# Optimization experiments

Measured on AMD Instinct MI355X. Metric: run time of the kernel, lower is better.

Reference implementation:

```python
import jax, jax.numpy as jnp
import numpy as np

NUM_ITERATIONS = 3

def _squash(s):
    # Original squash reduces over the trailing singleton dim -> elementwise.
    sn = s * s
    return sn * s / ((1.0 + sn) * jnp.sqrt(sn))

def setup_inputs() -> dict:
    key = jax.random.key(0)
    k1, k2 = jax.random.split(key)
    x = jax.random.normal(k1, (128, 1152, 8), dtype=jnp.float32)
    W = jax.random.normal(k2, (1, 1152, 16, 16, 8), dtype=jnp.float32)
    return {"x": x, "W": W}

def reference(x, W):
    # x: [B, R, I]; W: [1, R, C, O, I]
    Wr = W[0]  # [R, C, O, I]
    # u_hat = W @ x broadcast over capsules: [B, R, C, O]
    u_hat = jnp.einsum('rcoi,bri->brco', Wr, x)
    R, C = Wr.shape[0], Wr.shape[1]
    b = jnp.zeros((R, C), dtype=x.dtype)  # routing logits (shared across batch)
    v = None
    for it in range(NUM_ITERATIONS):
        # legacy F.softmax on [1,R,C,1] -> dim=1 == routes axis
        c = jax.nn.softmax(b, axis=0)  # [R, C]
        s = jnp.einsum('rc,brco->bco', c, u_hat)  # [B, C, O]
        v = _squash(s)
        if it < NUM_ITERATIONS - 1:
            # agreement: <u_hat, v> averaged over batch
            a = jnp.einsum('brco,bco->brc', u_hat, v).mean(axis=0)  # [R, C]
            b = b + a
    return v  # [B, C, O] == v_j.squeeze(1).squeeze(-1)
```

## Files before the change

### kernel.cpp

```cpp
#include <hip/hip_runtime.h>
#include <math.h>

#define B_   128
#define R_   1152
#define C_   16
#define O_   16
#define RS_  192
#define RCH_ 6

#define WS_SP   0
#define WS_V    6291456
#define WS_BLOG 6324224
#define WS_CW   6342656
#define WS_AB   6361088

__device__ __forceinline__ float squashf(float s) {
    return s * fabsf(s) / (1.0f + s * s);
}

__global__ void softmax_k(float* __restrict__ blog, const float* __restrict__ ab,
                          float* __restrict__ cw, int first) {
    const int c = blockIdx.x;
    const int t = threadIdx.x;
    __shared__ float red[256];

    float m = -1e30f;
    for (int r = t; r < R_; r += 256) {
        const float prev = first ? 0.f : blog[r * C_ + c];
        const float bl = prev + (ab[r * C_ + c] + ab[R_ * C_ + r * C_ + c]) * (1.0f / (float)B_);
        blog[r * C_ + c] = bl;
        m = fmaxf(m, bl);
    }
    red[t] = m; __syncthreads();
    for (int s = 128; s > 0; s >>= 1) {
        if (t < s) red[t] = fmaxf(red[t], red[t + s]);
        __syncthreads();
    }
    const float M = red[0]; __syncthreads();

    float e = 0.f;
    for (int r = t; r < R_; r += 256) e += __expf(blog[r * C_ + c] - M);
    red[t] = e; __syncthreads();
    for (int s = 128; s > 0; s >>= 1) {
        if (t < s) red[t] += red[t + s];
        __syncthreads();
    }
    const float inv = 1.0f / red[0];

    for (int r = t; r < R_; r += 256)
        cw[r * C_ + c] = __expf(blog[r * C_ + c] - M) * inv;
}

template <bool USECW>
__global__ __launch_bounds__(256) void gemm_s_k(const float* __restrict__ x,
                                                const float* __restrict__ W,
                                                const float* __restrict__ cw,
                                                float* __restrict__ sp) {
    const int bt  = blockIdx.x;
    const int rs  = blockIdx.y;
    const int t   = threadIdx.x;
    const int co4 = t & 63;
    const int b4  = t >> 6;
    const int c   = co4 >> 2;
    const int r0  = rs * RCH_;

    __shared__ float4 wl4[RCH_ * 520];
    __shared__ float4 xl4[16 * 2 * RCH_];

    const float4* __restrict__ X4 = (const float4*)x;
    const float4* __restrict__ W4 = (const float4*)W;

    #pragma unroll
    for (int kk = 0; kk < 12; ++kk) {
        const int u  = t + kk * 256;
        const int rr = u >> 9, j = u & 511;
        wl4[rr * 520 + (j & 7) * 65 + (j >> 3)] = W4[r0 * 512 + u];
    }
    if (t < 192) {
        const int bl = t / 12, rem = t % 12;
        xl4[t] = X4[((bt * 16 + bl) * R_ + r0) * 2 + rem];
    }
    __syncthreads();

    float acc[4][4];
    #pragma unroll
    for (int j = 0; j < 4; ++j)
        #pragma unroll
        for (int q = 0; q < 4; ++q) acc[j][q] = 0.f;

    #pragma unroll
    for (int rr = 0; rr < RCH_; ++rr) {
        const float cwv = USECW ? cw[(r0 + rr) * C_ + c] : (1.0f / (float)R_);
        const int wb = rr * 520 + co4;
        const float4 w0 = wl4[wb +   0], w1 = wl4[wb +  65];
        const float4 w2 = wl4[wb + 130], w3 = wl4[wb + 195];
        const float4 w4 = wl4[wb + 260], w5 = wl4[wb + 325];
        const float4 w6 = wl4[wb + 390], w7 = wl4[wb + 455];
        #pragma unroll
        for (int j = 0; j < 4; ++j) {
            const float4 xa = xl4[(b4 * 4 + j) * 12 + rr * 2];
            const float4 xb = xl4[(b4 * 4 + j) * 12 + rr * 2 + 1];
            const float d0 = w0.x*xa.x + w0.y*xa.y + w0.z*xa.z + w0.w*xa.w
                           + w1.x*xb.x + w1.y*xb.y + w1.z*xb.z + w1.w*xb.w;
            const float d1 = w2.x*xa.x + w2.y*xa.y + w2.z*xa.z + w2.w*xa.w
                           + w3.x*xb.x + w3.y*xb.y + w3.z*xb.z + w3.w*xb.w;
            const float d2 = w4.x*xa.x + w4.y*xa.y + w4.z*xa.z + w4.w*xa.w
                           + w5.x*xb.x + w5.y*xb.y + w5.z*xb.z + w5.w*xb.w;
            const float d3 = w6.x*xa.x + w6.y*xa.y + w6.z*xa.z + w6.w*xa.w
                           + w7.x*xb.x + w7.y*xb.y + w7.z*xb.z + w7.w*xb.w;
            acc[j][0] = fmaf(cwv, d0, acc[j][0]);
            acc[j][1] = fmaf(cwv, d1, acc[j][1]);
            acc[j][2] = fmaf(cwv, d2, acc[j][2]);
            acc[j][3] = fmaf(cwv, d3, acc[j][3]);
        }
    }

    float4* sp4 = (float4*)sp;
    #pragma unroll
    for (int j = 0; j < 4; ++j) {
        const int b = bt * 16 + b4 * 4 + j;
        float4 o4; o4.x = acc[j][0]; o4.y = acc[j][1]; o4.z = acc[j][2]; o4.w = acc[j][3];
        sp4[(rs * B_ + b) * 64 + co4] = o4;
    }
}

__global__ __launch_bounds__(1024) void reduce_squash_k(const float* __restrict__ sp,
                                                        float* __restrict__ outv) {
    const int t   = threadIdx.x;
    const int li  = t & 255;
    const int kq  = t >> 8;
    const int idx = blockIdx.x * 256 + li;
    const float* p = sp + (size_t)kq * (RS_ / 4) * 32768 + idx;
    float a0 = 0.f, a1 = 0.f, a2 = 0.f, a3 = 0.f;
    #pragma unroll 6
    for (int k = 0; k < RS_ / 4; k += 4) {
        a0 += p[(k + 0) * 32768];
        a1 += p[(k + 1) * 32768];
        a2 += p[(k + 2) * 32768];
        a3 += p[(k + 3) * 32768];
    }
    __shared__ float red[1024];
    red[t] = (a0 + a1) + (a2 + a3);
    __syncthreads();
    if (t < 256) {
        const float s = (red[t] + red[t + 256]) + (red[t + 512] + red[t + 768]);
        outv[idx] = squashf(s);
    }
}

__global__ __launch_bounds__(512) void a_k(const float* __restrict__ x,
                                           const float* __restrict__ W,
                                           const float* __restrict__ v,
                                           float* __restrict__ ab) {
    const int rg   = blockIdx.x >> 1;
    const int half = blockIdx.x & 1;
    const int r0   = rg * 4;
    const int b00  = half * 64;
    const int t    = threadIdx.x;
    const int w    = t >> 6, lane = t & 63;
    const int rr   = w & 3, sq = w >> 2;
    const int co4  = lane, c = lane >> 2;

    __shared__ float4 xl[64 * 8];
    __shared__ float4 wl[4 * 520];
    __shared__ float  red[128];
    const float4* __restrict__ X4 = (const float4*)x;
    const float4* __restrict__ V4 = (const float4*)v;
    const float4* __restrict__ W4 = (const float4*)W;

    #pragma unroll
    for (int kk = 0; kk < 4; ++kk) {
        const int u  = t + kk * 512;
        const int r2 = u >> 9, j = u & 511;
        wl[r2 * 520 + (j & 7) * 65 + (j >> 3)] = W4[r0 * 512 + u];
    }
    {
        const int bl = t >> 3, rem = t & 7;
        xl[t] = X4[((b00 + bl) * R_ + r0) * 2 + rem];
    }
    __syncthreads();

    float y[8][4];
    #pragma unroll
    for (int i = 0; i < 8; ++i)
        #pragma unroll
        for (int q = 0; q < 4; ++q) y[i][q] = 0.f;

    const int bbase = b00 + sq * 32;
    const int xbase = sq * 32;
    #pragma unroll 4
    for (int bb = 0; bb < 32; ++bb) {
        const float4 xa = xl[(xbase + bb) * 8 + rr * 2];
        const float4 xb = xl[(xbase + bb) * 8 + rr * 2 + 1];
        const float4 vv = V4[(bbase + bb) * 64 + co4];
        const float xs[8] = {xa.x, xa.y, xa.z, xa.w, xb.x, xb.y, xb.z, xb.w};
        #pragma unroll
        for (int i = 0; i < 8; ++i) {
            y[i][0] = fmaf(xs[i], vv.x, y[i][0]);
            y[i][1] = fmaf(xs[i], vv.y, y[i][1]);
            y[i][2] = fmaf(xs[i], vv.z, y[i][2]);
            y[i][3] = fmaf(xs[i], vv.w, y[i][3]);
        }
    }

    const int wb = rr * 520 + co4;
    float part = 0.f;
    #pragma unroll
    for (int q = 0; q < 4; ++q) {
        const float4 w0 = wl[wb + (2 * q) * 65];
        const float4 w1 = wl[wb + (2 * q + 1) * 65];
        part += w0.x*y[0][q] + w0.y*y[1][q] + w0.z*y[2][q] + w0.w*y[3][q]
              + w1.x*y[4][q] + w1.y*y[5][q] + w1.z*y[6][q] + w1.w*y[7][q];
    }
    part += __shfl_xor(part, 1);
    part += __shfl_xor(part, 2);
    if ((lane & 3) == 0) red[w * 16 + c] = part;
    __syncthreads();
    if (t < 64) {
        const int rr2 = t >> 4, cc = t & 15;
        ab[half * (R_ * C_) + (r0 + rr2) * C_ + cc] =
            red[rr2 * 16 + cc] + red[(rr2 + 4) * 16 + cc];
    }
}

extern "C" void kernel_launch(void* const* d_in, const int* in_sizes, int n_in,
                              void* d_out, int out_size, void* d_ws, size_t ws_size,
                              hipStream_t stream) {
    const float* x = (const float*)d_in[0];
    const float* W = (const float*)d_in[1];
    float* out = (float*)d_out;
    float* ws  = (float*)d_ws;

    float* sp   = ws + WS_SP;
    float* v    = ws + WS_V;
    float* blog = ws + WS_BLOG;
    float* cw   = ws + WS_CW;
    float* ab   = ws + WS_AB;

    gemm_s_k<false><<<dim3(8, RS_), 256, 0, stream>>>(x, W, cw, sp);
    reduce_squash_k<<<128, 1024, 0, stream>>>(sp, v);
    a_k<<<576, 512, 0, stream>>>(x, W, v, ab);

    softmax_k<<<C_, 256, 0, stream>>>(blog, ab, cw, 1);
    gemm_s_k<true><<<dim3(8, RS_), 256, 0, stream>>>(x, W, cw, sp);
    reduce_squash_k<<<128, 1024, 0, stream>>>(sp, v);
    a_k<<<576, 512, 0, stream>>>(x, W, v, ab);

    softmax_k<<<C_, 256, 0, stream>>>(blog, ab, cw, 0);
    gemm_s_k<true><<<dim3(8, RS_), 256, 0, stream>>>(x, W, cw, sp);
    reduce_squash_k<<<128, 1024, 0, stream>>>(sp, out);
}
```

Measured before the change: 192.9 us.

## Fuse softmax into gemm kernel, fold batch halves in agreement kernel

Removes the separate softmax kernel. Each gemm block now recomputes the column max and sum over the routing logits, then builds its own chunk of coefficients in shared memory. The agreement kernel covers the full batch per block and accumulates the logits directly, so the partial buffer and its merge step are gone. The gemm tile doubles to 32 batches per block and the reduce kernel is retuned. This cuts two launches per iteration and the single-block serial softmax, at the cost of every gemm block redundantly reading the whole logit array and fewer blocks overall.

```diff
diff --git a/kernel.cpp b/kernel.cpp
--- a/kernel.cpp
+++ b/kernel.cpp
@@ -11,61 +11,29 @@
 #define WS_SP   0
 #define WS_V    6291456
 #define WS_BLOG 6324224
-#define WS_CW   6342656
-#define WS_AB   6361088
 
 __device__ __forceinline__ float squashf(float s) {
     return s * fabsf(s) / (1.0f + s * s);
 }
 
-__global__ void softmax_k(float* __restrict__ blog, const float* __restrict__ ab,
-                          float* __restrict__ cw, int first) {
-    const int c = blockIdx.x;
-    const int t = threadIdx.x;
-    __shared__ float red[256];
-
-    float m = -1e30f;
-    for (int r = t; r < R_; r += 256) {
-        const float prev = first ? 0.f : blog[r * C_ + c];
-        const float bl = prev + (ab[r * C_ + c] + ab[R_ * C_ + r * C_ + c]) * (1.0f / (float)B_);
-        blog[r * C_ + c] = bl;
-        m = fmaxf(m, bl);
-    }
-    red[t] = m; __syncthreads();
-    for (int s = 128; s > 0; s >>= 1) {
-        if (t < s) red[t] = fmaxf(red[t], red[t + s]);
-        __syncthreads();
-    }
-    const float M = red[0]; __syncthreads();
-
-    float e = 0.f;
-    for (int r = t; r < R_; r += 256) e += __expf(blog[r * C_ + c] - M);
-    red[t] = e; __syncthreads();
-    for (int s = 128; s > 0; s >>= 1) {
-        if (t < s) red[t] += red[t + s];
-        __syncthreads();
-    }
-    const float inv = 1.0f / red[0];
-
-    for (int r = t; r < R_; r += 256)
-        cw[r * C_ + c] = __expf(blog[r * C_ + c] - M) * inv;
-}
-
-template <bool USECW>
+template <bool PRE>
 __global__ __launch_bounds__(256) void gemm_s_k(const float* __restrict__ x,
                                                 const float* __restrict__ W,
-                                                const float* __restrict__ cw,
+                                                const float* __restrict__ blog,
                                                 float* __restrict__ sp) {
     const int bt  = blockIdx.x;
     const int rs  = blockIdx.y;
     const int t   = threadIdx.x;
     const int co4 = t & 63;
-    const int b4  = t >> 6;
+    const int b8  = t >> 6;
     const int c   = co4 >> 2;
     const int r0  = rs * RCH_;
 
     __shared__ float4 wl4[RCH_ * 520];
-    __shared__ float4 xl4[16 * 2 * RCH_];
+    __shared__ float4 xl4[32 * 2 * RCH_];
+    __shared__ float4 part[16];
+    __shared__ float  colmax[16], colinv[16];
+    __shared__ float  cwl[RCH_ * 16];
 
     const float4* __restrict__ X4 = (const float4*)x;
     const float4* __restrict__ W4 = (const float4*)W;
@@ -76,30 +44,93 @@
         const int rr = u >> 9, j = u & 511;
         wl4[rr * 520 + (j & 7) * 65 + (j >> 3)] = W4[r0 * 512 + u];
     }
-    if (t < 192) {
-        const int bl = t / 12, rem = t % 12;
-        xl4[t] = X4[((bt * 16 + bl) * R_ + r0) * 2 + rem];
-    }
-    __syncthreads();
-
-    float acc[4][4];
-    #pragma unroll
-    for (int j = 0; j < 4; ++j)
+    {
+        int u = t;
+        { const int bl = u / 12, rem = u % 12;
+          xl4[u] = X4[((bt * 32 + bl) * R_ + r0) * 2 + rem]; }
+        u = t + 256;
+        if (u < 384) {
+            const int bl = u / 12, rem = u % 12;
+            xl4[u] = X4[((bt * 32 + bl) * R_ + r0) * 2 + rem];
+        }
+    }
+
+    if (PRE) {
+        const float4* BL4 = (const float4*)blog;
+        const int g = t & 3;
+        float4 m4; m4.x = -1e30f; m4.y = -1e30f; m4.z = -1e30f; m4.w = -1e30f;
+        #pragma unroll
+        for (int i = 0; i < 18; ++i) {
+            const float4 bv = BL4[i * 256 + t];
+            m4.x = fmaxf(m4.x, bv.x); m4.y = fmaxf(m4.y, bv.y);
+            m4.z = fmaxf(m4.z, bv.z); m4.w = fmaxf(m4.w, bv.w);
+        }
+        #pragma unroll
+        for (int d = 4; d < 64; d <<= 1) {
+            m4.x = fmaxf(m4.x, __shfl_xor(m4.x, d));
+            m4.y = fmaxf(m4.y, __shfl_xor(m4.y, d));
+            m4.z = fmaxf(m4.z, __shfl_xor(m4.z, d));
+            m4.w = fmaxf(m4.w, __shfl_xor(m4.w, d));
+        }
+        if ((t & 63) < 4) part[(t >> 6) * 4 + g] = m4;
+        __syncthreads();
+        if (t < 4) {
+            const float4 a = part[t], b = part[4 + t], cc4 = part[8 + t], d = part[12 + t];
+            colmax[t * 4 + 0] = fmaxf(fmaxf(a.x, b.x), fmaxf(cc4.x, d.x));
+            colmax[t * 4 + 1] = fmaxf(fmaxf(a.y, b.y), fmaxf(cc4.y, d.y));
+            colmax[t * 4 + 2] = fmaxf(fmaxf(a.z, b.z), fmaxf(cc4.z, d.z));
+            colmax[t * 4 + 3] = fmaxf(fmaxf(a.w, b.w), fmaxf(cc4.w, d.w));
+        }
+        __syncthreads();
+        const float Mx = colmax[g * 4 + 0], My = colmax[g * 4 + 1];
+        const float Mz = colmax[g * 4 + 2], Mw = colmax[g * 4 + 3];
+        float4 e4; e4.x = 0.f; e4.y = 0.f; e4.z = 0.f; e4.w = 0.f;
+        #pragma unroll
+        for (int i = 0; i < 18; ++i) {
+            const float4 bv = BL4[i * 256 + t];
+            e4.x += __expf(bv.x - Mx); e4.y += __expf(bv.y - My);
+            e4.z += __expf(bv.z - Mz); e4.w += __expf(bv.w - Mw);
+        }
+        #pragma unroll
+        for (int d = 4; d < 64; d <<= 1) {
+            e4.x += __shfl_xor(e4.x, d); e4.y += __shfl_xor(e4.y, d);
+            e4.z += __shfl_xor(e4.z, d); e4.w += __shfl_xor(e4.w, d);
+        }
+        if ((t & 63) < 4) part[(t >> 6) * 4 + g] = e4;
+        __syncthreads();
+        if (t < 4) {
+            const float4 a = part[t], b = part[4 + t], cc4 = part[8 + t], d = part[12 + t];
+            colinv[t * 4 + 0] = 1.0f / ((a.x + b.x) + (cc4.x + d.x));
+            colinv[t * 4 + 1] = 1.0f / ((a.y + b.y) + (cc4.y + d.y));
+            colinv[t * 4 + 2] = 1.0f / ((a.z + b.z) + (cc4.z + d.z));
+            colinv[t * 4 + 3] = 1.0f / ((a.w + b.w) + (cc4.w + d.w));
+        }
+        __syncthreads();
+        if (t < RCH_ * 16) {
+            const int rl = t >> 4, cc = t & 15;
+            cwl[t] = __expf(blog[(r0 + rl) * 16 + cc] - colmax[cc]) * colinv[cc];
+        }
+    }
+    __syncthreads();
+
+    float acc[8][4];
+    #pragma unroll
+    for (int j = 0; j < 8; ++j)
         #pragma unroll
         for (int q = 0; q < 4; ++q) acc[j][q] = 0.f;
 
     #pragma unroll
     for (int rr = 0; rr < RCH_; ++rr) {
-        const float cwv = USECW ? cw[(r0 + rr) * C_ + c] : (1.0f / (float)R_);
+        const float cwv = PRE ? cwl[rr * 16 + c] : (1.0f / (float)R_);
         const int wb = rr * 520 + co4;
         const float4 w0 = wl4[wb +   0], w1 = wl4[wb +  65];
         const float4 w2 = wl4[wb + 130], w3 = wl4[wb + 195];
         const float4 w4 = wl4[wb + 260], w5 = wl4[wb + 325];
         const float4 w6 = wl4[wb + 390], w7 = wl4[wb + 455];
         #pragma unroll
-        for (int j = 0; j < 4; ++j) {
-            const float4 xa = xl4[(b4 * 4 + j) * 12 + rr * 2];
-            const float4 xb = xl4[(b4 * 4 + j) * 12 + rr * 2 + 1];
+        for (int j = 0; j < 8; ++j) {
+            const float4 xa = xl4[(b8 * 8 + j) * 12 + rr * 2];
+            const float4 xb = xl4[(b8 * 8 + j) * 12 + rr * 2 + 1];
             const float d0 = w0.x*xa.x + w0.y*xa.y + w0.z*xa.z + w0.w*xa.w
                            + w1.x*xb.x + w1.y*xb.y + w1.z*xb.z + w1.w*xb.w;
             const float d1 = w2.x*xa.x + w2.y*xa.y + w2.z*xa.z + w2.w*xa.w
@@ -117,51 +148,49 @@
 
     float4* sp4 = (float4*)sp;
     #pragma unroll
-    for (int j = 0; j < 4; ++j) {
-        const int b = bt * 16 + b4 * 4 + j;
+    for (int j = 0; j < 8; ++j) {
+        const int b = bt * 32 + b8 * 8 + j;
         float4 o4; o4.x = acc[j][0]; o4.y = acc[j][1]; o4.z = acc[j][2]; o4.w = acc[j][3];
         sp4[(rs * B_ + b) * 64 + co4] = o4;
     }
 }
 
-__global__ __launch_bounds__(1024) void reduce_squash_k(const float* __restrict__ sp,
-                                                        float* __restrict__ outv) {
+__global__ __launch_bounds__(512) void reduce_squash_k(const float* __restrict__ sp,
+                                                       float* __restrict__ outv) {
     const int t   = threadIdx.x;
-    const int li  = t & 255;
-    const int kq  = t >> 8;
-    const int idx = blockIdx.x * 256 + li;
-    const float* p = sp + (size_t)kq * (RS_ / 4) * 32768 + idx;
+    const int li  = t & 127;
+    const int kq  = t >> 7;
+    const int idx = blockIdx.x * 128 + li;
+    const float* p = sp + (size_t)kq * 48 * 32768 + idx;
     float a0 = 0.f, a1 = 0.f, a2 = 0.f, a3 = 0.f;
     #pragma unroll 6
-    for (int k = 0; k < RS_ / 4; k += 4) {
+    for (int k = 0; k < 48; k += 4) {
         a0 += p[(k + 0) * 32768];
         a1 += p[(k + 1) * 32768];
         a2 += p[(k + 2) * 32768];
         a3 += p[(k + 3) * 32768];
     }
-    __shared__ float red[1024];
+    __shared__ float red[512];
     red[t] = (a0 + a1) + (a2 + a3);
     __syncthreads();
-    if (t < 256) {
-        const float s = (red[t] + red[t + 256]) + (red[t + 512] + red[t + 768]);
+    if (t < 128) {
+        const float s = (red[t] + red[t + 128]) + (red[t + 256] + red[t + 384]);
         outv[idx] = squashf(s);
     }
 }
 
+template <bool FIRST>
 __global__ __launch_bounds__(512) void a_k(const float* __restrict__ x,
                                            const float* __restrict__ W,
                                            const float* __restrict__ v,
-                                           float* __restrict__ ab) {
-    const int rg   = blockIdx.x >> 1;
-    const int half = blockIdx.x & 1;
-    const int r0   = rg * 4;
-    const int b00  = half * 64;
-    const int t    = threadIdx.x;
-    const int w    = t >> 6, lane = t & 63;
-    const int rr   = w & 3, sq = w >> 2;
-    const int co4  = lane, c = lane >> 2;
-
-    __shared__ float4 xl[64 * 8];
+                                           float* __restrict__ blog) {
+    const int r0 = blockIdx.x * 4;
+    const int t  = threadIdx.x;
+    const int w  = t >> 6, lane = t & 63;
+    const int rr = w & 3, half = w >> 2;
+    const int co4 = lane, c = lane >> 2;
+
+    __shared__ float4 xl[128 * 8];
     __shared__ float4 wl[4 * 520];
     __shared__ float  red[128];
     const float4* __restrict__ X4 = (const float4*)x;
@@ -174,9 +203,11 @@
         const int r2 = u >> 9, j = u & 511;
         wl[r2 * 520 + (j & 7) * 65 + (j >> 3)] = W4[r0 * 512 + u];
     }
-    {
-        const int bl = t >> 3, rem = t & 7;
-        xl[t] = X4[((b00 + bl) * R_ + r0) * 2 + rem];
+    #pragma unroll
+    for (int kk = 0; kk < 2; ++kk) {
+        const int u = t + kk * 512;
+        const int b = u >> 3, rem = u & 7;
+        xl[u] = X4[(b * R_ + r0) * 2 + rem];
     }
     __syncthreads();
 
@@ -186,13 +217,13 @@
         #pragma unroll
         for (int q = 0; q < 4; ++q) y[i][q] = 0.f;
 
-    const int bbase = b00 + sq * 32;
-    const int xbase = sq * 32;
+    const int b0 = half * 64;
     #pragma unroll 4
-    for (int bb = 0; bb < 32; ++bb) {
-        const float4 xa = xl[(xbase + bb) * 8 + rr * 2];
-        const float4 xb = xl[(xbase + bb) * 8 + rr * 2 + 1];
-        const float4 vv = V4[(bbase + bb) * 64 + co4];
+    for (int bb = 0; bb < 64; ++bb) {
+        const int b = b0 + bb;
+        const float4 xa = xl[b * 8 + rr * 2];
+        const float4 xb = xl[b * 8 + rr * 2 + 1];
+        const float4 vv = V4[b * 64 + co4];
         const float xs[8] = {xa.x, xa.y, xa.z, xa.w, xb.x, xb.y, xb.z, xb.w};
         #pragma unroll
         for (int i = 0; i < 8; ++i) {
@@ -218,8 +249,9 @@
     __syncthreads();
     if (t < 64) {
         const int rr2 = t >> 4, cc = t & 15;
-        ab[half * (R_ * C_) + (r0 + rr2) * C_ + cc] =
-            red[rr2 * 16 + cc] + red[(rr2 + 4) * 16 + cc];
+        const float val = (red[rr2 * 16 + cc] + red[(rr2 + 4) * 16 + cc]) * (1.0f / (float)B_);
+        const int idx = (r0 + rr2) * 16 + cc;
+        blog[idx] = FIRST ? val : (blog[idx] + val);
     }
 }
 
@@ -234,19 +266,15 @@
     float* sp   = ws + WS_SP;
     float* v    = ws + WS_V;
     float* blog = ws + WS_BLOG;
-    float* cw   = ws + WS_CW;
-    float* ab   = ws + WS_AB;
-
-    gemm_s_k<false><<<dim3(8, RS_), 256, 0, stream>>>(x, W, cw, sp);
-    reduce_squash_k<<<128, 1024, 0, stream>>>(sp, v);
-    a_k<<<576, 512, 0, stream>>>(x, W, v, ab);
-
-    softmax_k<<<C_, 256, 0, stream>>>(blog, ab, cw, 1);
-    gemm_s_k<true><<<dim3(8, RS_), 256, 0, stream>>>(x, W, cw, sp);
-    reduce_squash_k<<<128, 1024, 0, stream>>>(sp, v);
-    a_k<<<576, 512, 0, stream>>>(x, W, v, ab);
-
-    softmax_k<<<C_, 256, 0, stream>>>(blog, ab, cw, 0);
-    gemm_s_k<true><<<dim3(8, RS_), 256, 0, stream>>>(x, W, cw, sp);
-    reduce_squash_k<<<128, 1024, 0, stream>>>(sp, out);
-}
+
+    gemm_s_k<false><<<dim3(4, RS_), 256, 0, stream>>>(x, W, blog, sp);
+    reduce_squash_k<<<256, 512, 0, stream>>>(sp, v);
+    a_k<true><<<288, 512, 0, stream>>>(x, W, v, blog);
+
+    gemm_s_k<true><<<dim3(4, RS_), 256, 0, stream>>>(x, W, blog, sp);
+    reduce_squash_k<<<256, 512, 0, stream>>>(sp, v);
+    a_k<false><<<288, 512, 0, stream>>>(x, W, v, blog);
+
+    gemm_s_k<true><<<dim3(4, RS_), 256, 0, stream>>>(x, W, blog, sp);
+    reduce_squash_k<<<256, 512, 0, stream>>>(sp, out);
+}
```

Result: no change. 196.1 us (+1.7%).
